# Performance work log

Hardware: AMD Instinct MI355X
Metric: run time of the kernel (lower is better)

The kernel has to match this reference:

```python
import jax, jax.numpy as jnp
import numpy as np

EPS = 1e-5

@jax.custom_vjp
def ste_quantize(w):
    # abs-mean scale, round, clamp to {-1, 0, 1}
    scale = jnp.maximum(jnp.mean(jnp.abs(w)), EPS)
    return jnp.clip(jnp.round(w / scale), -1.0, 1.0)

def _ste_fwd(w):
    return ste_quantize(w), None

def _ste_bwd(_, g):
    # straight-through: gradient passes unchanged
    return (g,)

ste_quantize.defvjp(_ste_fwd, _ste_bwd)


def setup_inputs() -> dict:
    key = jax.random.key(0)
    k1, k2 = jax.random.split(key)
    x = jax.random.normal(k1, (8, 8192, 1024), dtype=jnp.float32)       # [B, S, in]
    weight = jax.random.normal(k2, (1024, 1024), dtype=jnp.float32) * 0.02  # [out, in]
    return {"x": x, "weight": weight}


def reference(x, weight):
    w_ternary = ste_quantize(weight)                         # [out, in] in {-1,0,1}
    scale = jnp.maximum(jnp.mean(jnp.abs(weight)), EPS)      # scalar (differentiable path)
    # F.linear(x, w_ternary * scale): out = x @ (w_ternary*scale)^T
    return jnp.einsum('bsi,oi->bso', x, w_ternary * scale)
```

## Files before the change

kernel.cpp:

```cpp
#include <hip/hip_runtime.h>
#include <stdint.h>

#define K_DIM 1024
#define N_DIM 1024
#define M_MAX 65536

#define BM 256
#define BN 256
#define BK 32
#define NKT (K_DIM / BK)
#define NBUF 3
#define A_TILE (BM * BK)
#define B_TILE (BN * BK)

typedef __attribute__((ext_vector_type(8))) __bf16 bf16x8;
typedef __attribute__((ext_vector_type(4))) float f32x4;

__device__ __align__(16) unsigned short g_wq[N_DIM * K_DIM];
__device__ __align__(16) unsigned short g_xq[(size_t)M_MAX * K_DIM];
__device__ double g_partial[256];
__device__ float g_scale;

__device__ __forceinline__ unsigned int pack_bf16(float hi, float lo) {
  return __builtin_amdgcn_perm(__float_as_uint(hi), __float_as_uint(lo), 0x07060302u);
}

__global__ void absum_kernel(const float* __restrict__ w) {
  const int tid = threadIdx.x, bid = blockIdx.x;
  const float4* w4 = (const float4*)w;
  double s = 0.0;
#pragma unroll
  for (int i = 0; i < 4; i++) {
    float4 v = w4[bid * 1024 + i * 256 + tid];
    s += (double)fabsf(v.x) + (double)fabsf(v.y) + (double)fabsf(v.z) + (double)fabsf(v.w);
  }
#pragma unroll
  for (int o = 32; o > 0; o >>= 1) s += __shfl_down(s, o);
  __shared__ double sm[4];
  if ((tid & 63) == 0) sm[tid >> 6] = s;
  __syncthreads();
  if (tid == 0) g_partial[bid] = sm[0] + sm[1] + sm[2] + sm[3];
}

__global__ void scale_kernel() {
  const int tid = threadIdx.x;
  double v = g_partial[tid];
#pragma unroll
  for (int o = 32; o > 0; o >>= 1) v += __shfl_down(v, o);
  __shared__ double sm[4];
  if ((tid & 63) == 0) sm[tid >> 6] = v;
  __syncthreads();
  if (tid == 0) {
    double total = sm[0] + sm[1] + sm[2] + sm[3];
    double mean = total * (1.0 / 1048576.0);
    g_scale = (float)fmax(mean, 1e-5);
  }
}

__global__ void quant_kernel(const float* __restrict__ w) {
  const int idx = blockIdx.x * 256 + threadIdx.x;
  const float s = g_scale;
  float4 v = ((const float4*)w)[idx];
  float q0 = fminf(1.f, fmaxf(-1.f, rintf(v.x / s)));
  float q1 = fminf(1.f, fmaxf(-1.f, rintf(v.y / s)));
  float q2 = fminf(1.f, fmaxf(-1.f, rintf(v.z / s)));
  float q3 = fminf(1.f, fmaxf(-1.f, rintf(v.w / s)));
  ushort4 o;
  o.x = (unsigned short)(__float_as_uint(q0) >> 16);
  o.y = (unsigned short)(__float_as_uint(q1) >> 16);
  o.z = (unsigned short)(__float_as_uint(q2) >> 16);
  o.w = (unsigned short)(__float_as_uint(q3) >> 16);
  ((ushort4*)g_wq)[idx] = o;
}

__global__ __launch_bounds__(256) void convert_x(const float* __restrict__ x) {
  const size_t t = (size_t)blockIdx.x * 256 + threadIdx.x;
  const float4* x4 = (const float4*)x;
  float4 a = x4[t * 2];
  float4 b = x4[t * 2 + 1];
  uint4 o;
  o.x = pack_bf16(a.y, a.x);
  o.y = pack_bf16(a.w, a.z);
  o.z = pack_bf16(b.y, b.x);
  o.w = pack_bf16(b.w, b.z);
  ((uint4*)g_xq)[t] = o;
}

__global__ __launch_bounds__(512, 2) void bitlinear_gemm(float* __restrict__ C) {
  __shared__ __align__(16) unsigned short As[NBUF * A_TILE];
  __shared__ __align__(16) unsigned short Bs[NBUF * B_TILE];

  const int tid  = threadIdx.x;
  const int lane = tid & 63;
  const int wave = tid >> 6;
  const int wm   = wave >> 2;
  const int wn   = wave & 3;
  const int lm   = lane & 15;
  const int lq   = lane >> 4;

  const int b       = blockIdx.x;
  const int cpx     = (int)(gridDim.x >> 3);
  const int logical = (b & 7) * cpx + (b >> 3);
  const int mt      = logical >> 2;
  const int nt      = logical & 3;
  const int m0      = mt * BM;
  const int n0      = nt * BN;

  f32x4 acc[8][4];
#pragma unroll
  for (int i = 0; i < 8; i++)
#pragma unroll
    for (int j = 0; j < 4; j++) acc[i][j] = (f32x4){0.f, 0.f, 0.f, 0.f};

  const int cswz = ((lane & 3) ^ ((lane >> 3) & 3)) * 8;
  const unsigned short* aSrc =
      g_xq + (size_t)(m0 + wave * 32 + (lane >> 2)) * K_DIM + cswz;
  const unsigned short* bSrc =
      g_wq + (size_t)(n0 + wave * 32 + (lane >> 2)) * K_DIM + cswz;
  const int ldsDst = wave * 32 * BK;

#define STAGE_A(tt, bb)                                                        \
  do {                                                                         \
    const unsigned short* s_ = aSrc + (tt) * BK;                               \
    unsigned short* d_ = &As[(bb) * A_TILE + ldsDst];                          \
    __builtin_amdgcn_global_load_lds(                                          \
        (const __attribute__((address_space(1))) unsigned int*)s_,             \
        (__attribute__((address_space(3))) unsigned int*)d_, 16, 0, 0);        \
    __builtin_amdgcn_global_load_lds(                                          \
        (const __attribute__((address_space(1))) unsigned int*)(s_ + 16 * K_DIM), \
        (__attribute__((address_space(3))) unsigned int*)(d_ + 16 * BK), 16, 0, 0); \
  } while (0)

#define STAGE_B(tt, bb)                                                        \
  do {                                                                         \
    const unsigned short* s_ = bSrc + (tt) * BK;                               \
    unsigned short* d_ = &Bs[(bb) * B_TILE + ldsDst];                          \
    __builtin_amdgcn_global_load_lds(                                          \
        (const __attribute__((address_space(1))) unsigned int*)s_,             \
        (__attribute__((address_space(3))) unsigned int*)d_, 16, 0, 0);        \
    __builtin_amdgcn_global_load_lds(                                          \
        (const __attribute__((address_space(1))) unsigned int*)(s_ + 16 * K_DIM), \
        (__attribute__((address_space(3))) unsigned int*)(d_ + 16 * BK), 16, 0, 0); \
  } while (0)

  const int xorc = (((lm >> 1) & 3) ^ lq) * 8;
  const int aRd  = (wm * 128 + lm) * BK + xorc;
  const int bRd  = (wn * 64 + lm) * BK + xorc;

  STAGE_A(0, 0);
  STAGE_B(0, 0);
  STAGE_A(1, 1);
  STAGE_B(1, 1);

  int buf = 0;
#pragma unroll 1
  for (int t = 0; t < NKT; ++t) {
    if (t == NKT - 1)
      asm volatile("s_waitcnt vmcnt(0)\n\ts_barrier" ::: "memory");
    else
      asm volatile("s_waitcnt vmcnt(4)\n\ts_barrier" ::: "memory");

    const unsigned short* Ab = &As[buf * A_TILE + aRd];
    const unsigned short* Bb = &Bs[buf * B_TILE + bRd];
    const int nbuf = (buf + 2 >= NBUF) ? buf + 2 - NBUF : buf + 2;

    bf16x8 bfr[4], af[4];
#pragma unroll
    for (int nf = 0; nf < 4; ++nf) bfr[nf] = *(const bf16x8*)(Bb + nf * 16 * BK);
#pragma unroll
    for (int mf = 0; mf < 4; ++mf) af[mf] = *(const bf16x8*)(Ab + mf * 16 * BK);

    if (t + 2 < NKT) STAGE_A(t + 2, nbuf);

    asm volatile("s_barrier" ::: "memory");

    __builtin_amdgcn_s_setprio(1);
#pragma unroll
    for (int mf = 0; mf < 4; ++mf)
#pragma unroll
      for (int nf = 0; nf < 4; ++nf)
        acc[mf][nf] = __builtin_amdgcn_mfma_f32_16x16x32_bf16(af[mf], bfr[nf],
                                                              acc[mf][nf], 0, 0, 0);
    __builtin_amdgcn_s_setprio(0);

    asm volatile("s_barrier" ::: "memory");

    bf16x8 af2[4];
#pragma unroll
    for (int mf = 0; mf < 4; ++mf)
      af2[mf] = *(const bf16x8*)(Ab + (mf + 4) * 16 * BK);

    if (t + 2 < NKT) STAGE_B(t + 2, nbuf);

    asm volatile("s_barrier" ::: "memory");

    __builtin_amdgcn_s_setprio(1);
#pragma unroll
    for (int mf = 0; mf < 4; ++mf)
#pragma unroll
      for (int nf = 0; nf < 4; ++nf)
        acc[mf + 4][nf] = __builtin_amdgcn_mfma_f32_16x16x32_bf16(
            af2[mf], bfr[nf], acc[mf + 4][nf], 0, 0, 0);
    __builtin_amdgcn_s_setprio(0);

    buf = (buf + 1 == NBUF) ? 0 : buf + 1;
  }
#undef STAGE_A
#undef STAGE_B

  const float s    = g_scale;
  const int   crow = m0 + wm * 128 + lq * 4;
  const int   ccol = n0 + wn * 64 + lm;
#pragma unroll
  for (int mf = 0; mf < 8; ++mf) {
#pragma unroll
    for (int nf = 0; nf < 4; ++nf) {
#pragma unroll
      for (int r = 0; r < 4; ++r) {
        C[(size_t)(crow + mf * 16 + r) * N_DIM + (ccol + nf * 16)] =
            acc[mf][nf][r] * s;
      }
    }
  }
}

extern "C" void kernel_launch(void* const* d_in, const int* in_sizes, int n_in,
                              void* d_out, int out_size, void* d_ws, size_t ws_size,
                              hipStream_t stream) {
  const float* x = (const float*)d_in[0];
  const float* w = (const float*)d_in[1];
  float* out = (float*)d_out;
  const int M = in_sizes[0] / K_DIM;

  hipLaunchKernelGGL(absum_kernel, dim3(256), dim3(256), 0, stream, w);
  hipLaunchKernelGGL(scale_kernel, dim3(1), dim3(256), 0, stream);
  hipLaunchKernelGGL(quant_kernel, dim3(1024), dim3(256), 0, stream, w);
  hipLaunchKernelGGL(convert_x, dim3((unsigned)((size_t)M * K_DIM / 8 / 256)), dim3(256), 0,
                     stream, x);
  hipLaunchKernelGGL(bitlinear_gemm,
                     dim3((unsigned)(((size_t)M / BM) * (N_DIM / BN))),
                     dim3(512), 0, stream, out);
}
```

Before: 628.1 us.

## Deepen GEMM LDS ring to four stages with register-prefetched fragments

The GEMM main loop moves from a 3-buffer LDS ring with prefetch distance 2 to a 4-buffer ring with prefetch distance 3, unrolled by two k-steps. A and B fragments for the next k-tile are now read from LDS into registers during the current tile's MFMA phase, so LDS reads overlap with matrix math instead of stalling at the start of each iteration. The goal is to hide global-to-LDS and LDS-to-register latency better. In exchange, LDS use rises to 128KB per block, register pressure grows from the extra fragment set, and the hand-tuned vmcnt counts must match the new issue order exactly.

```diff
diff --git a/kernel.cpp b/kernel.cpp
--- a/kernel.cpp
+++ b/kernel.cpp
@@ -9,7 +9,7 @@
 #define BN 256
 #define BK 32
 #define NKT (K_DIM / BK)
-#define NBUF 3
+#define NBUF 4
 #define A_TILE (BM * BK)
 #define B_TILE (BN * BK)
 
@@ -151,59 +151,124 @@
   STAGE_B(0, 0);
   STAGE_A(1, 1);
   STAGE_B(1, 1);
-
-  int buf = 0;
+  STAGE_A(2, 2);
+  STAGE_B(2, 2);
+  asm volatile("s_waitcnt vmcnt(8)\n\ts_barrier" ::: "memory");
+
+  bf16x8 afE[4], bfE[4], afO[4], bfO[4];
+  {
+    const unsigned short* Ab0 = &As[aRd];
+    const unsigned short* Bb0 = &Bs[bRd];
+#pragma unroll
+    for (int mf = 0; mf < 4; ++mf) afE[mf] = *(const bf16x8*)(Ab0 + mf * 16 * BK);
+#pragma unroll
+    for (int nf = 0; nf < 4; ++nf) bfE[nf] = *(const bf16x8*)(Bb0 + nf * 16 * BK);
+  }
+
 #pragma unroll 1
-  for (int t = 0; t < NKT; ++t) {
-    if (t == NKT - 1)
-      asm volatile("s_waitcnt vmcnt(0)\n\ts_barrier" ::: "memory");
-    else
-      asm volatile("s_waitcnt vmcnt(4)\n\ts_barrier" ::: "memory");
-
-    const unsigned short* Ab = &As[buf * A_TILE + aRd];
-    const unsigned short* Bb = &Bs[buf * B_TILE + bRd];
-    const int nbuf = (buf + 2 >= NBUF) ? buf + 2 - NBUF : buf + 2;
-
-    bf16x8 bfr[4], af[4];
-#pragma unroll
-    for (int nf = 0; nf < 4; ++nf) bfr[nf] = *(const bf16x8*)(Bb + nf * 16 * BK);
-#pragma unroll
-    for (int mf = 0; mf < 4; ++mf) af[mf] = *(const bf16x8*)(Ab + mf * 16 * BK);
-
-    if (t + 2 < NKT) STAGE_A(t + 2, nbuf);
-
-    asm volatile("s_barrier" ::: "memory");
-
-    __builtin_amdgcn_s_setprio(1);
-#pragma unroll
-    for (int mf = 0; mf < 4; ++mf)
-#pragma unroll
-      for (int nf = 0; nf < 4; ++nf)
-        acc[mf][nf] = __builtin_amdgcn_mfma_f32_16x16x32_bf16(af[mf], bfr[nf],
-                                                              acc[mf][nf], 0, 0, 0);
-    __builtin_amdgcn_s_setprio(0);
-
-    asm volatile("s_barrier" ::: "memory");
-
-    bf16x8 af2[4];
-#pragma unroll
-    for (int mf = 0; mf < 4; ++mf)
-      af2[mf] = *(const bf16x8*)(Ab + (mf + 4) * 16 * BK);
-
-    if (t + 2 < NKT) STAGE_B(t + 2, nbuf);
-
-    asm volatile("s_barrier" ::: "memory");
-
-    __builtin_amdgcn_s_setprio(1);
-#pragma unroll
-    for (int mf = 0; mf < 4; ++mf)
-#pragma unroll
-      for (int nf = 0; nf < 4; ++nf)
-        acc[mf + 4][nf] = __builtin_amdgcn_mfma_f32_16x16x32_bf16(
-            af2[mf], bfr[nf], acc[mf + 4][nf], 0, 0, 0);
-    __builtin_amdgcn_s_setprio(0);
-
-    buf = (buf + 1 == NBUF) ? 0 : buf + 1;
+  for (int tt = 0; tt < NKT; tt += 2) {
+    const int cb = tt & 3;
+
+    {
+      const unsigned short* Ab = &As[cb * A_TILE + aRd];
+      const unsigned short* Bb = &Bs[cb * B_TILE + bRd];
+
+      bf16x8 a2[4];
+#pragma unroll
+      for (int mf = 0; mf < 4; ++mf)
+        a2[mf] = *(const bf16x8*)(Ab + (mf + 4) * 16 * BK);
+      if (tt < 29) STAGE_A(tt + 3, cb ^ 3);
+      if (tt < 30)
+        asm volatile("s_waitcnt vmcnt(6)\n\ts_barrier" ::: "memory");
+      else
+        asm volatile("s_waitcnt vmcnt(0)\n\ts_barrier" ::: "memory");
+
+      __builtin_amdgcn_s_setprio(1);
+#pragma unroll
+      for (int mf = 0; mf < 4; ++mf)
+#pragma unroll
+        for (int nf = 0; nf < 4; ++nf)
+          acc[mf][nf] = __builtin_amdgcn_mfma_f32_16x16x32_bf16(
+              afE[mf], bfE[nf], acc[mf][nf], 0, 0, 0);
+      __builtin_amdgcn_s_setprio(0);
+      asm volatile("s_barrier" ::: "memory");
+
+      {
+        const int cn = cb + 1;
+        const unsigned short* AbN = &As[cn * A_TILE + aRd];
+        const unsigned short* BbN = &Bs[cn * B_TILE + bRd];
+#pragma unroll
+        for (int mf = 0; mf < 4; ++mf)
+          afO[mf] = *(const bf16x8*)(AbN + mf * 16 * BK);
+#pragma unroll
+        for (int nf = 0; nf < 4; ++nf)
+          bfO[nf] = *(const bf16x8*)(BbN + nf * 16 * BK);
+      }
+      if (tt < 29) STAGE_B(tt + 3, cb ^ 3);
+      asm volatile("s_barrier" ::: "memory");
+
+      __builtin_amdgcn_s_setprio(1);
+#pragma unroll
+      for (int mf = 0; mf < 4; ++mf)
+#pragma unroll
+        for (int nf = 0; nf < 4; ++nf)
+          acc[mf + 4][nf] = __builtin_amdgcn_mfma_f32_16x16x32_bf16(
+              a2[mf], bfE[nf], acc[mf + 4][nf], 0, 0, 0);
+      __builtin_amdgcn_s_setprio(0);
+      asm volatile("s_barrier" ::: "memory");
+    }
+
+    {
+      const int cu = cb + 1;
+      const unsigned short* Ab = &As[cu * A_TILE + aRd];
+      const unsigned short* Bb = &Bs[cu * B_TILE + bRd];
+
+      bf16x8 a2[4];
+#pragma unroll
+      for (int mf = 0; mf < 4; ++mf)
+        a2[mf] = *(const bf16x8*)(Ab + (mf + 4) * 16 * BK);
+      if (tt < 28) STAGE_A(tt + 4, cb);
+      if (tt < 28)
+        asm volatile("s_waitcnt vmcnt(6)\n\ts_barrier" ::: "memory");
+      else if (tt < 30)
+        asm volatile("s_waitcnt vmcnt(4)\n\ts_barrier" ::: "memory");
+      else
+        asm volatile("s_waitcnt vmcnt(0)\n\ts_barrier" ::: "memory");
+
+      __builtin_amdgcn_s_setprio(1);
+#pragma unroll
+      for (int mf = 0; mf < 4; ++mf)
+#pragma unroll
+        for (int nf = 0; nf < 4; ++nf)
+          acc[mf][nf] = __builtin_amdgcn_mfma_f32_16x16x32_bf16(
+              afO[mf], bfO[nf], acc[mf][nf], 0, 0, 0);
+      __builtin_amdgcn_s_setprio(0);
+      asm volatile("s_barrier" ::: "memory");
+
+      if (tt < 30) {
+        const int cn = cb ^ 2;
+        const unsigned short* AbN = &As[cn * A_TILE + aRd];
+        const unsigned short* BbN = &Bs[cn * B_TILE + bRd];
+#pragma unroll
+        for (int mf = 0; mf < 4; ++mf)
+          afE[mf] = *(const bf16x8*)(AbN + mf * 16 * BK);
+#pragma unroll
+        for (int nf = 0; nf < 4; ++nf)
+          bfE[nf] = *(const bf16x8*)(BbN + nf * 16 * BK);
+      }
+      if (tt < 28) STAGE_B(tt + 4, cb);
+      asm volatile("s_barrier" ::: "memory");
+
+      __builtin_amdgcn_s_setprio(1);
+#pragma unroll
+      for (int mf = 0; mf < 4; ++mf)
+#pragma unroll
+        for (int nf = 0; nf < 4; ++nf)
+          acc[mf + 4][nf] = __builtin_amdgcn_mfma_f32_16x16x32_bf16(
+              a2[mf], bfO[nf], acc[mf + 4][nf], 0, 0, 0);
+      __builtin_amdgcn_s_setprio(0);
+      asm volatile("s_barrier" ::: "memory");
+    }
   }
 #undef STAGE_A
 #undef STAGE_B
```

New measurement: 629.1 us. About the same (+0.2%).
